# Performance work log

Measured on AMD Instinct MI355X. Metric: run time of the kernel, lower is better.

## Reference

```python
import jax, jax.numpy as jnp
import numpy as np

N_NODES = 100000
N_EDGES = 3200000
D_IN = 128
D_OUT = 128


def setup_inputs() -> dict:
    key = jax.random.key(0)
    k1, k2, k3, k4, k5 = jax.random.split(key, 5)
    x = jax.random.normal(k1, (N_NODES, D_IN), dtype=jnp.float32)
    edge_index = jax.random.randint(k2, (2, N_EDGES), 0, N_NODES, dtype=jnp.int64)
    edge_weight = jax.random.uniform(k3, (N_EDGES,), dtype=jnp.float32)
    W = jax.random.normal(k4, (D_IN, D_OUT), dtype=jnp.float32) / np.sqrt(D_IN)
    b = jax.random.normal(k5, (D_OUT,), dtype=jnp.float32)
    return {"x": x, "edge_index": edge_index, "edge_weight": edge_weight, "W": W, "b": b}


def reference(x, edge_index, edge_weight, W, b):
    # GCNConv: add self-loops (weight 1), symmetric deg^{-1/2} normalization,
    # linear transform, scatter-add aggregation source -> target, + bias.
    N = x.shape[0]
    src, dst = edge_index[0], edge_index[1]
    loops = jnp.arange(N, dtype=edge_index.dtype)
    src_f = jnp.concatenate([src, loops])
    dst_f = jnp.concatenate([dst, loops])
    w_f = jnp.concatenate([edge_weight, jnp.ones((N,), dtype=edge_weight.dtype)])
    # degree over target nodes (PyG gcn_norm with flow source_to_target)
    deg = jax.ops.segment_sum(w_f, dst_f, num_segments=N)
    deg_inv_sqrt = jnp.where(deg > 0, jax.lax.rsqrt(deg), 0.0)
    norm = deg_inv_sqrt[src_f] * w_f * deg_inv_sqrt[dst_f]  # [E+N]
    h = x @ W  # [N, D_OUT]
    msgs = h[src_f] * norm[:, None]  # gather + scale, [E+N, D_OUT]
    out = jax.ops.segment_sum(msgs, dst_f, num_segments=N)  # scatter-add
    return out + b
```

## Files before the change

### kernel.cpp

```cpp
#include <hip/hip_runtime.h>

#define NN 100000
#define NE 3200000
#define D  128
#define NBUCK 391

typedef __attribute__((ext_vector_type(8))) short bf16x8;
typedef __attribute__((ext_vector_type(4))) float f32x4;
typedef __attribute__((ext_vector_type(2))) float f32x2;

__device__ __forceinline__ float bf2f(unsigned int u) {
    union { unsigned int i; float f; } v; v.i = u << 16; return v.f;
}
__device__ __forceinline__ float bits2f(unsigned int u) {
    union { unsigned int i; float f; } v; v.i = u; return v.f;
}
__device__ __forceinline__ unsigned int f2bf(float f) {
    union { float f; unsigned int i; } v; v.f = f;
    unsigned int u = v.i;
    return (u + 0x7fffu + ((u >> 16) & 1u)) >> 16;
}

__global__ __launch_bounds__(512) void zero_detect_kernel(const int* __restrict__ ei,
        int* __restrict__ flag, int* __restrict__ gcnt) {
    int t = threadIdx.x;
    if (t < NBUCK) gcnt[t] = 0;
    if (t < 64) {
        int v = ei[2 * t + 1];
        unsigned long long ball = __ballot(v != 0);
        if (t == 0) flag[0] = (ball == 0ull) ? 1 : 0;
    }
}

__global__ __launch_bounds__(256) void count1_kernel(const int* __restrict__ ei,
        int* __restrict__ gcnt, int* __restrict__ blockbase, const int* __restrict__ flag) {
    __shared__ int h[NBUCK + 1];
    int t = threadIdx.x, b = blockIdx.x;
    int s = flag[0];
    for (int j = t; j <= NBUCK; j += 256) h[j] = 0;
    __syncthreads();
    long e0 = (long)b * 8192;
    for (int it = 0; it < 32; ++it) {
        long e = e0 + it * 256 + t;
        if (e < NE) {
            int d = s ? (int)((const long*)ei)[NE + e] : ei[NE + e];
            atomicAdd(&h[d >> 8], 1);
        }
    }
    __syncthreads();
    for (int j = t; j < NBUCK; j += 256) {
        int bb = atomicAdd(&gcnt[j], h[j]);
        blockbase[b * NBUCK + j] = bb;
    }
}

__global__ __launch_bounds__(512) void scatter1_kernel(const int* __restrict__ ei,
        const float* __restrict__ ew, const int* __restrict__ gcnt,
        const int* __restrict__ blockbase, const int* __restrict__ flag,
        unsigned long long* __restrict__ tmp, int* __restrict__ gbase) {
    __shared__ int gb[512];
    __shared__ int bb[NBUCK + 1];
    __shared__ int cur[NBUCK + 1];
    int t = threadIdx.x, b = blockIdx.x;
    int s = flag[0];
    gb[t] = (t < NBUCK) ? gcnt[t] : 0;
    if (t <= NBUCK) cur[t] = 0;
    if (t < NBUCK) bb[t] = blockbase[b * NBUCK + t];
    __syncthreads();
    for (int off = 1; off < 512; off <<= 1) {
        int v = (t >= off) ? gb[t - off] : 0;
        __syncthreads();
        gb[t] += v;
        __syncthreads();
    }
    if (b == 0) {
        if (t < NBUCK) gbase[t] = (t > 0) ? gb[t - 1] : 0;
        if (t == 0) gbase[NBUCK] = NE;
    }
    long e0 = (long)b * 8192;
    for (int it = 0; it < 16; ++it) {
        long e = e0 + it * 512 + t;
        if (e < NE) {
            int src, dst;
            if (s) { src = (int)((const long*)ei)[e]; dst = (int)((const long*)ei)[NE + e]; }
            else   { src = ei[e];                     dst = ei[NE + e]; }
            float w = ew[e];
            int bkt = dst >> 8, dlow = dst & 255;
            int r = atomicAdd(&cur[bkt], 1);
            int base = (bkt > 0) ? gb[bkt - 1] : 0;
            unsigned int word = ((unsigned int)src << 15) | (f2bf(w) >> 1);
            tmp[base + bb[bkt] + r] = ((unsigned long long)(unsigned int)dlow << 32) | word;
        }
    }
}

__global__ __launch_bounds__(256) void build2_kernel(const unsigned long long* __restrict__ tmp,
        const int* __restrict__ gbase, int* __restrict__ row_ptr, unsigned int* __restrict__ csr) {
    __shared__ int hist[256], excl[256], cur[256];
    int t = threadIdx.x, k = blockIdx.x;
    int base = gbase[k], endb = gbase[k + 1];
    hist[t] = 0; cur[t] = 0;
    __syncthreads();
    for (int i = base + t; i < endb; i += 256) {
        unsigned long long v = tmp[i];
        atomicAdd(&hist[(int)(v >> 32)], 1);
    }
    __syncthreads();
    excl[t] = hist[t];
    __syncthreads();
    for (int off = 1; off < 256; off <<= 1) {
        int v = (t >= off) ? excl[t - off] : 0;
        __syncthreads();
        excl[t] += v;
        __syncthreads();
    }
    int ex = excl[t] - hist[t];
    int node = k * 256 + t;
    if (node < NN) row_ptr[node] = base + ex;
    if (node == NN - 1) row_ptr[NN] = NE;
    __syncthreads();
    excl[t] = ex;
    __syncthreads();
    for (int i = base + t; i < endb; i += 256) {
        unsigned long long v = tmp[i];
        int dl = (int)(v >> 32);
        int r = atomicAdd(&cur[dl], 1);
        csr[base + excl[dl] + r] = (unsigned int)v;
    }
}

__global__ __launch_bounds__(256) void disr_kernel(const int* __restrict__ row_ptr,
        const unsigned int* __restrict__ csr, float* __restrict__ dis) {
    int n = blockIdx.x * 4 + (threadIdx.x >> 6);
    int l = threadIdx.x & 63;
    int beg = row_ptr[n], end = row_ptr[n + 1];
    float s = 0.f;
    for (int e = beg + l; e < end; e += 64)
        s += bf2f((csr[e] & 0x7fffu) << 1);
    for (int off = 32; off; off >>= 1) s += __shfl_down(s, off);
    if (l == 0) dis[n] = rsqrtf(1.0f + s);
}

__global__ __launch_bounds__(256) void mgemm_kernel(const float* __restrict__ x,
        const float* __restrict__ W, const float* __restrict__ dis,
        unsigned short* __restrict__ hb) {
    __shared__ unsigned short WT[16 * 128 * 8];
    int t = threadIdx.x;
    {
        int n = t & 127, half = t >> 7;
        for (int it = 0; it < 8; ++it) {
            int kb = half * 8 + it;
            union { unsigned short s[8]; uint4 v; } pk;
#pragma unroll
            for (int j = 0; j < 8; ++j)
                pk.s[j] = (unsigned short)f2bf(W[(kb * 8 + j) * D + n]);
            *(uint4*)&WT[(kb * 128 + n) * 8] = pk.v;
        }
    }
    __syncthreads();
    int l = t & 63, w = t >> 6;
    int q = l >> 4, m = l & 15;
    long mbase = (long)blockIdx.x * 128 + w * 32;
    long r0 = mbase + m;      if (r0 > NN - 1) r0 = NN - 1;
    long r1 = mbase + 16 + m; if (r1 > NN - 1) r1 = NN - 1;
    const float* a0p = x + r0 * D + q * 8;
    const float* a1p = x + r1 * D + q * 8;
    f32x4 acc[2][8];
#pragma unroll
    for (int mt = 0; mt < 2; ++mt)
#pragma unroll
        for (int nt = 0; nt < 8; ++nt) acc[mt][nt] = (f32x4){0.f, 0.f, 0.f, 0.f};
#pragma unroll
    for (int kc = 0; kc < 4; ++kc) {
        float4 va0 = *(const float4*)(a0p + kc * 32);
        float4 va1 = *(const float4*)(a0p + kc * 32 + 4);
        float4 vb0 = *(const float4*)(a1p + kc * 32);
        float4 vb1 = *(const float4*)(a1p + kc * 32 + 4);
        union { unsigned short s[8]; bf16x8 v; } ua, ub;
        ua.s[0] = (unsigned short)f2bf(va0.x); ua.s[1] = (unsigned short)f2bf(va0.y);
        ua.s[2] = (unsigned short)f2bf(va0.z); ua.s[3] = (unsigned short)f2bf(va0.w);
        ua.s[4] = (unsigned short)f2bf(va1.x); ua.s[5] = (unsigned short)f2bf(va1.y);
        ua.s[6] = (unsigned short)f2bf(va1.z); ua.s[7] = (unsigned short)f2bf(va1.w);
        ub.s[0] = (unsigned short)f2bf(vb0.x); ub.s[1] = (unsigned short)f2bf(vb0.y);
        ub.s[2] = (unsigned short)f2bf(vb0.z); ub.s[3] = (unsigned short)f2bf(vb0.w);
        ub.s[4] = (unsigned short)f2bf(vb1.x); ub.s[5] = (unsigned short)f2bf(vb1.y);
        ub.s[6] = (unsigned short)f2bf(vb1.z); ub.s[7] = (unsigned short)f2bf(vb1.w);
        const bf16x8* bp = (const bf16x8*)WT + (kc * 4 + q) * 128 + m;
#pragma unroll
        for (int nt = 0; nt < 8; ++nt) {
            bf16x8 bfr = bp[nt * 16];
            acc[0][nt] = __builtin_amdgcn_mfma_f32_16x16x32_bf16(ua.v, bfr, acc[0][nt], 0, 0, 0);
            acc[1][nt] = __builtin_amdgcn_mfma_f32_16x16x32_bf16(ub.v, bfr, acc[1][nt], 0, 0, 0);
        }
    }
#pragma unroll
    for (int mt = 0; mt < 2; ++mt) {
        long rowbase = mbase + mt * 16;
#pragma unroll
        for (int r = 0; r < 4; ++r) {
            long row = rowbase + q * 4 + r;
            float dsc = dis[(row < NN) ? row : (NN - 1)];
#pragma unroll
            for (int nt = 0; nt < 8; ++nt)
                if (row < NN)
                    hb[row * D + nt * 16 + m] = (unsigned short)f2bf(acc[mt][nt][r] * dsc);
        }
    }
}

__global__ __launch_bounds__(256) void pull_kernel(const unsigned int* __restrict__ hb,
        const float* __restrict__ dis, const int* __restrict__ row_ptr,
        const unsigned int* __restrict__ csr, const float2* __restrict__ bias2,
        float* __restrict__ out) {
    int t = blockIdx.x * 256 + threadIdx.x;
    int n = t >> 6, l = t & 63;
    float dn = dis[n];
    unsigned int a = hb[n * 64 + l];
    float accx = bits2f(a << 16);
    float accy = bits2f(a & 0xffff0000u);
    int e = row_ptr[n], end = row_ptr[n + 1];
    for (; e + 7 < end; e += 8) {
        unsigned int c[8];
#pragma unroll
        for (int j = 0; j < 8; ++j) c[j] = __builtin_nontemporal_load(csr + e + j);
        int s_[8];
#pragma unroll
        for (int j = 0; j < 8; ++j) s_[j] = c[j] >> 15;
        unsigned int u[8];
#pragma unroll
        for (int j = 0; j < 8; ++j) u[j] = hb[s_[j] * 64 + l];
#pragma unroll
        for (int j = 0; j < 8; ++j) {
            float m = bits2f(c[j] << 17);
            accx += bits2f(u[j] << 16) * m;
            accy += bits2f(u[j] & 0xffff0000u) * m;
        }
    }
    for (; e + 1 < end; e += 2) {
        unsigned int c0 = __builtin_nontemporal_load(csr + e);
        unsigned int c1 = __builtin_nontemporal_load(csr + e + 1);
        int s0 = c0 >> 15, s1 = c1 >> 15;
        unsigned int u0 = hb[s0 * 64 + l];
        unsigned int u1 = hb[s1 * 64 + l];
        float m0 = bits2f(c0 << 17), m1 = bits2f(c1 << 17);
        accx += bits2f(u0 << 16) * m0; accy += bits2f(u0 & 0xffff0000u) * m0;
        accx += bits2f(u1 << 16) * m1; accy += bits2f(u1 & 0xffff0000u) * m1;
    }
    if (e < end) {
        unsigned int c0 = __builtin_nontemporal_load(csr + e);
        int s0 = c0 >> 15;
        unsigned int u0 = hb[s0 * 64 + l];
        float m0 = bits2f(c0 << 17);
        accx += bits2f(u0 << 16) * m0; accy += bits2f(u0 & 0xffff0000u) * m0;
    }
    float2 bv = bias2[l];
    f32x2 r;
    r.x = accx * dn + bv.x;
    r.y = accy * dn + bv.y;
    __builtin_nontemporal_store(r, (f32x2*)out + ((size_t)n * 64 + l));
}

extern "C" void kernel_launch(void* const* d_in, const int* in_sizes, int n_in,
                              void* d_out, int out_size, void* d_ws, size_t ws_size,
                              hipStream_t stream) {
    const float* x  = (const float*)d_in[0];
    const int*   ei = (const int*)d_in[1];
    const float* ew = (const float*)d_in[2];
    const float* W  = (const float*)d_in[3];
    const float* b  = (const float*)d_in[4];
    float* out = (float*)d_out;

    unsigned long long* tmp = (unsigned long long*)d_ws;
    unsigned short*     hb  = (unsigned short*)d_ws;
    unsigned int*       csr = (unsigned int*)((char*)d_ws + (size_t)NE * 8);
    float*              dis = (float*)(csr + NE);
    int*            row_ptr = (int*)(dis + NN);
    int*            gcnt    = row_ptr + NN + 1;
    int*            gbase   = gcnt + NBUCK;
    int*            flag    = gbase + NBUCK + 1;
    int*          blockbase = flag + 1;

    zero_detect_kernel<<<1, 512, 0, stream>>>(ei, flag, gcnt);
    count1_kernel<<<NBUCK, 256, 0, stream>>>(ei, gcnt, blockbase, flag);
    scatter1_kernel<<<NBUCK, 512, 0, stream>>>(ei, ew, gcnt, blockbase, flag, tmp, gbase);
    build2_kernel<<<NBUCK, 256, 0, stream>>>(tmp, gbase, row_ptr, csr);
    disr_kernel<<<NN / 4, 256, 0, stream>>>(row_ptr, csr, dis);
    mgemm_kernel<<<(NN + 127) / 128, 256, 0, stream>>>(x, W, dis, hb);
    pull_kernel<<<(NN * 64) / 256, 256, 0, stream>>>((const unsigned int*)hb, dis, row_ptr, csr,
                                                     (const float2*)b, (float*)out);
}
```

Measured before the change: 382.3 us.

## Rework CSR build with finer buckets, more blocks, and fused degree computation

```diff
diff --git a/kernel.cpp b/kernel.cpp
--- a/kernel.cpp
+++ b/kernel.cpp
@@ -3,7 +3,9 @@
 #define NN 100000
 #define NE 3200000
 #define D  128
-#define NBUCK 391
+#define NBUCK 782
+#define EPB 2048
+#define NBLK ((NE + EPB - 1) / EPB)
 
 typedef __attribute__((ext_vector_type(8))) short bf16x8;
 typedef __attribute__((ext_vector_type(4))) float f32x4;
@@ -21,7 +23,7 @@
     return (u + 0x7fffu + ((u >> 16) & 1u)) >> 16;
 }
 
-__global__ __launch_bounds__(512) void zero_detect_kernel(const int* __restrict__ ei,
+__global__ __launch_bounds__(1024) void zero_detect_kernel(const int* __restrict__ ei,
         int* __restrict__ flag, int* __restrict__ gcnt) {
     int t = threadIdx.x;
     if (t < NBUCK) gcnt[t] = 0;
@@ -33,93 +35,114 @@
 }
 
 __global__ __launch_bounds__(256) void count1_kernel(const int* __restrict__ ei,
-        int* __restrict__ gcnt, int* __restrict__ blockbase, const int* __restrict__ flag) {
-    __shared__ int h[NBUCK + 1];
+        int* __restrict__ gcnt, unsigned short* __restrict__ blockbase,
+        const int* __restrict__ flag) {
+    __shared__ int h[NBUCK];
     int t = threadIdx.x, b = blockIdx.x;
     int s = flag[0];
-    for (int j = t; j <= NBUCK; j += 256) h[j] = 0;
-    __syncthreads();
-    long e0 = (long)b * 8192;
-    for (int it = 0; it < 32; ++it) {
+    for (int j = t; j < NBUCK; j += 256) h[j] = 0;
+    __syncthreads();
+    long e0 = (long)b * EPB;
+#pragma unroll
+    for (int it = 0; it < EPB / 256; ++it) {
         long e = e0 + it * 256 + t;
         if (e < NE) {
             int d = s ? (int)((const long*)ei)[NE + e] : ei[NE + e];
-            atomicAdd(&h[d >> 8], 1);
+            atomicAdd(&h[d >> 7], 1);
         }
     }
     __syncthreads();
     for (int j = t; j < NBUCK; j += 256) {
-        int bb = atomicAdd(&gcnt[j], h[j]);
-        blockbase[b * NBUCK + j] = bb;
-    }
-}
-
-__global__ __launch_bounds__(512) void scatter1_kernel(const int* __restrict__ ei,
-        const float* __restrict__ ew, const int* __restrict__ gcnt,
-        const int* __restrict__ blockbase, const int* __restrict__ flag,
-        unsigned long long* __restrict__ tmp, int* __restrict__ gbase) {
-    __shared__ int gb[512];
-    __shared__ int bb[NBUCK + 1];
-    __shared__ int cur[NBUCK + 1];
+        int v = h[j];
+        unsigned short bb = 0;
+        if (v) bb = (unsigned short)atomicAdd(&gcnt[j], v);
+        blockbase[(size_t)b * NBUCK + j] = bb;
+    }
+}
+
+__global__ __launch_bounds__(1024) void scanb_kernel(const int* __restrict__ gcnt,
+        int* __restrict__ gbase) {
+    __shared__ int s[1024];
+    int t = threadIdx.x;
+    s[t] = (t < NBUCK) ? gcnt[t] : 0;
+    __syncthreads();
+    for (int off = 1; off < 1024; off <<= 1) {
+        int v = (t >= off) ? s[t - off] : 0;
+        __syncthreads();
+        s[t] += v;
+        __syncthreads();
+    }
+    if (t < NBUCK) gbase[t] = (t > 0) ? s[t - 1] : 0;
+    if (t == 0) gbase[NBUCK] = NE;
+}
+
+__global__ __launch_bounds__(256) void scatter1_kernel(const int* __restrict__ ei,
+        const float* __restrict__ ew, const int* __restrict__ gbase,
+        const unsigned short* __restrict__ blockbase, const int* __restrict__ flag,
+        unsigned long long* __restrict__ tmp) {
+    __shared__ int gb[NBUCK];
+    __shared__ unsigned short bbs[NBUCK];
+    __shared__ int cur[NBUCK];
     int t = threadIdx.x, b = blockIdx.x;
     int s = flag[0];
-    gb[t] = (t < NBUCK) ? gcnt[t] : 0;
-    if (t <= NBUCK) cur[t] = 0;
-    if (t < NBUCK) bb[t] = blockbase[b * NBUCK + t];
-    __syncthreads();
-    for (int off = 1; off < 512; off <<= 1) {
-        int v = (t >= off) ? gb[t - off] : 0;
-        __syncthreads();
-        gb[t] += v;
-        __syncthreads();
-    }
-    if (b == 0) {
-        if (t < NBUCK) gbase[t] = (t > 0) ? gb[t - 1] : 0;
-        if (t == 0) gbase[NBUCK] = NE;
-    }
-    long e0 = (long)b * 8192;
-    for (int it = 0; it < 16; ++it) {
-        long e = e0 + it * 512 + t;
+    for (int j = t; j < NBUCK; j += 256) {
+        gb[j] = gbase[j];
+        bbs[j] = blockbase[(size_t)b * NBUCK + j];
+        cur[j] = 0;
+    }
+    __syncthreads();
+    long e0 = (long)b * EPB;
+#pragma unroll
+    for (int it = 0; it < EPB / 256; ++it) {
+        long e = e0 + it * 256 + t;
         if (e < NE) {
             int src, dst;
             if (s) { src = (int)((const long*)ei)[e]; dst = (int)((const long*)ei)[NE + e]; }
             else   { src = ei[e];                     dst = ei[NE + e]; }
             float w = ew[e];
-            int bkt = dst >> 8, dlow = dst & 255;
+            int bkt = dst >> 7, dlow = dst & 127;
             int r = atomicAdd(&cur[bkt], 1);
-            int base = (bkt > 0) ? gb[bkt - 1] : 0;
             unsigned int word = ((unsigned int)src << 15) | (f2bf(w) >> 1);
-            tmp[base + bb[bkt] + r] = ((unsigned long long)(unsigned int)dlow << 32) | word;
+            tmp[gb[bkt] + (int)bbs[bkt] + r] =
+                ((unsigned long long)(unsigned int)dlow << 32) | word;
         }
     }
 }
 
 __global__ __launch_bounds__(256) void build2_kernel(const unsigned long long* __restrict__ tmp,
-        const int* __restrict__ gbase, int* __restrict__ row_ptr, unsigned int* __restrict__ csr) {
-    __shared__ int hist[256], excl[256], cur[256];
+        const int* __restrict__ gbase, int* __restrict__ row_ptr, unsigned int* __restrict__ csr,
+        float* __restrict__ dis) {
+    __shared__ int hist[128], excl[128], cur[128];
+    __shared__ float wsum[128];
     int t = threadIdx.x, k = blockIdx.x;
     int base = gbase[k], endb = gbase[k + 1];
-    hist[t] = 0; cur[t] = 0;
+    if (t < 128) { hist[t] = 0; cur[t] = 0; wsum[t] = 0.f; }
     __syncthreads();
     for (int i = base + t; i < endb; i += 256) {
         unsigned long long v = tmp[i];
-        atomicAdd(&hist[(int)(v >> 32)], 1);
-    }
-    __syncthreads();
-    excl[t] = hist[t];
-    __syncthreads();
-    for (int off = 1; off < 256; off <<= 1) {
-        int v = (t >= off) ? excl[t - off] : 0;
+        int dl = (int)(v >> 32);
+        atomicAdd(&hist[dl], 1);
+        atomicAdd(&wsum[dl], bf2f(((unsigned int)v & 0x7fffu) << 1));
+    }
+    __syncthreads();
+    if (t < 128) excl[t] = hist[t];
+    __syncthreads();
+    for (int off = 1; off < 128; off <<= 1) {
+        int v = (t >= off && t < 128) ? excl[t - off] : 0;
         __syncthreads();
-        excl[t] += v;
+        if (t < 128) excl[t] += v;
         __syncthreads();
     }
-    int ex = excl[t] - hist[t];
-    int node = k * 256 + t;
-    if (node < NN) row_ptr[node] = base + ex;
-    if (node == NN - 1) row_ptr[NN] = NE;
-    __syncthreads();
-    excl[t] = ex;
+    if (t < 128) {
+        int ex = excl[t] - hist[t];
+        int node = k * 128 + t;
+        if (node < NN) {
+            row_ptr[node] = base + ex;
+            dis[node] = rsqrtf(1.0f + wsum[t]);
+        }
+        if (node == NN - 1) row_ptr[NN] = NE;
+        excl[t] = ex;
+    }
     __syncthreads();
     for (int i = base + t; i < endb; i += 256) {
         unsigned long long v = tmp[i];
@@ -127,18 +150,6 @@
         int r = atomicAdd(&cur[dl], 1);
         csr[base + excl[dl] + r] = (unsigned int)v;
     }
-}
-
-__global__ __launch_bounds__(256) void disr_kernel(const int* __restrict__ row_ptr,
-        const unsigned int* __restrict__ csr, float* __restrict__ dis) {
-    int n = blockIdx.x * 4 + (threadIdx.x >> 6);
-    int l = threadIdx.x & 63;
-    int beg = row_ptr[n], end = row_ptr[n + 1];
-    float s = 0.f;
-    for (int e = beg + l; e < end; e += 64)
-        s += bf2f((csr[e] & 0x7fffu) << 1);
-    for (int off = 32; off; off >>= 1) s += __shfl_down(s, off);
-    if (l == 0) dis[n] = rsqrtf(1.0f + s);
 }
 
 __global__ __launch_bounds__(256) void mgemm_kernel(const float* __restrict__ x,
@@ -278,13 +289,13 @@
     int*            gcnt    = row_ptr + NN + 1;
     int*            gbase   = gcnt + NBUCK;
     int*            flag    = gbase + NBUCK + 1;
-    int*          blockbase = flag + 1;
-
-    zero_detect_kernel<<<1, 512, 0, stream>>>(ei, flag, gcnt);
-    count1_kernel<<<NBUCK, 256, 0, stream>>>(ei, gcnt, blockbase, flag);
-    scatter1_kernel<<<NBUCK, 512, 0, stream>>>(ei, ew, gcnt, blockbase, flag, tmp, gbase);
-    build2_kernel<<<NBUCK, 256, 0, stream>>>(tmp, gbase, row_ptr, csr);
-    disr_kernel<<<NN / 4, 256, 0, stream>>>(row_ptr, csr, dis);
+    unsigned short* blockbase = (unsigned short*)(flag + 1);
+
+    zero_detect_kernel<<<1, 1024, 0, stream>>>(ei, flag, gcnt);
+    count1_kernel<<<NBLK, 256, 0, stream>>>(ei, gcnt, blockbase, flag);
+    scanb_kernel<<<1, 1024, 0, stream>>>(gcnt, gbase);
+    scatter1_kernel<<<NBLK, 256, 0, stream>>>(ei, ew, gbase, blockbase, flag, tmp);
+    build2_kernel<<<NBUCK, 256, 0, stream>>>(tmp, gbase, row_ptr, csr, dis);
     mgemm_kernel<<<(NN + 127) / 128, 256, 0, stream>>>(x, W, dis, hb);
     pull_kernel<<<(NN * 64) / 256, 256, 0, stream>>>((const unsigned int*)hb, dis, row_ptr, csr,
                                                      (const float2*)b, (float*)out);
```

After: 442.5 us. +15.7%, slower.
